# Kernel optimization log

Hardware: AMD Instinct MI355X
Metric: run time of the kernel (lower is better)

The kernel has to match this reference:

```python
import jax, jax.numpy as jnp
import numpy as np

COMMITMENT_COST = 0.25
K = 512  # code_book_dim
D = 64   # embedding_dim
N = 262144


def setup_inputs() -> dict:
    key = jax.random.key(0)
    k1, k2 = jax.random.split(key)
    inputs = jax.random.normal(k1, (N, D), dtype=jnp.float32)
    # torch init: uniform_(-1/K, 1/K)
    codebook = jax.random.uniform(k2, (K, D), dtype=jnp.float32, minval=-1.0 / K, maxval=1.0 / K)
    return {"inputs": inputs, "codebook": codebook}


def reference(inputs, codebook):
    flat = inputs  # [N, D]
    x_sq = jnp.sum(flat * flat, axis=1, keepdims=True)          # [N, 1]
    e_sq = jnp.sum(codebook * codebook, axis=1)[None, :]        # [1, K]
    distances = x_sq + e_sq - 2.0 * flat @ codebook.T           # [N, K]
    encoding_indices = jnp.argmin(distances, axis=1)            # [N]
    quantized = codebook[encoding_indices]                      # [N, D]

    e_latent_loss = jnp.mean((jax.lax.stop_gradient(quantized) - flat) ** 2)
    q_latent_loss = jnp.mean((quantized - jax.lax.stop_gradient(flat)) ** 2)
    loss = q_latent_loss + COMMITMENT_COST * e_latent_loss

    # training-mode straight-through estimator
    quantized_st = flat + jax.lax.stop_gradient(quantized - flat)
    return loss, quantized_st, encoding_indices
```

## Files before the change

### kernel.cpp

```cpp
#include <hip/hip_runtime.h>
#include <hip/hip_bf16.h>

#define N_ROWS 262144
#define DIM 64
#define KC 512
#define BLK 512
#define RPT 2
#define LDS_FLOATS (KC * DIM + KC)


__device__ __forceinline__ float np_sumsq64(const float* a) {
#pragma clang fp contract(off)
    float r[8];
#pragma unroll
    for (int j = 0; j < 8; ++j) r[j] = a[j] * a[j];
#pragma unroll
    for (int i = 8; i < 64; i += 8)
#pragma unroll
        for (int j = 0; j < 8; ++j) r[j] = r[j] + a[i + j] * a[i + j];
    return ((r[0] + r[1]) + (r[2] + r[3])) + ((r[4] + r[5]) + (r[6] + r[7]));
}

__global__ void esq_kernel(const float* __restrict__ cb, float* __restrict__ esq) {
    int k = blockIdx.x * blockDim.x + threadIdx.x;
    if (k < KC) esq[k] = np_sumsq64(cb + k * DIM);
}

__global__ __launch_bounds__(BLK)
__attribute__((amdgpu_waves_per_eu(2, 2)))
void vq_kernel(
    const float* __restrict__ x, const float* __restrict__ cb,
    const float* __restrict__ esq_g, float* __restrict__ out,
    float* __restrict__ loss_acc)
{
    extern __shared__ float smem[];
    float* cbs  = smem;
    float* esql = smem + KC * DIM;

    const int tid  = threadIdx.x;
    const int lane = tid & 63;
    const int row0 = blockIdx.x * (BLK * RPT) + tid;
    const int row1 = row0 + BLK;

    {
        const float4* g4 = reinterpret_cast<const float4*>(cb);
        float4*       s4 = reinterpret_cast<float4*>(cbs);
#pragma unroll
        for (int i = 0; i < (KC * DIM / 4) / BLK; ++i)
            s4[tid + i * BLK] = g4[tid + i * BLK];
        if (tid < KC) esql[tid] = esq_g[tid];
    }

    float xr0[DIM], xr1[DIM];
    {
        const float4* xv0 = reinterpret_cast<const float4*>(x + (size_t)row0 * DIM);
        const float4* xv1 = reinterpret_cast<const float4*>(x + (size_t)row1 * DIM);
#pragma unroll
        for (int j = 0; j < DIM / 4; ++j) {
            float4 v0 = xv0[j], v1 = xv1[j];
            xr0[4 * j + 0] = v0.x; xr0[4 * j + 1] = v0.y;
            xr0[4 * j + 2] = v0.z; xr0[4 * j + 3] = v0.w;
            xr1[4 * j + 0] = v1.x; xr1[4 * j + 1] = v1.y;
            xr1[4 * j + 2] = v1.z; xr1[4 * j + 3] = v1.w;
        }
    }

    const float xsq0 = np_sumsq64(xr0);
    const float xsq1 = np_sumsq64(xr1);

    __syncthreads();

    float best0 = 3.4e38f, best1 = 3.4e38f;
    int bidx0 = 0, bidx1 = 0;
#pragma unroll 1
    for (int k = 0; k < KC; k += 2) {
        const float4* ea = reinterpret_cast<const float4*>(cbs + k * DIM);
        const float4* eb = ea + DIM / 4;
        float dot00 = 0.f, dot01 = 0.f, dot10 = 0.f, dot11 = 0.f;
#pragma unroll
        for (int c = 0; c < DIM / 4; ++c) {
            const float4 a = ea[c];
            const float4 b = eb[c];
            dot00 = fmaf(xr0[4 * c + 0], a.x, dot00);
            dot01 = fmaf(xr0[4 * c + 0], b.x, dot01);
            dot10 = fmaf(xr1[4 * c + 0], a.x, dot10);
            dot11 = fmaf(xr1[4 * c + 0], b.x, dot11);
            dot00 = fmaf(xr0[4 * c + 1], a.y, dot00);
            dot01 = fmaf(xr0[4 * c + 1], b.y, dot01);
            dot10 = fmaf(xr1[4 * c + 1], a.y, dot10);
            dot11 = fmaf(xr1[4 * c + 1], b.y, dot11);
            dot00 = fmaf(xr0[4 * c + 2], a.z, dot00);
            dot01 = fmaf(xr0[4 * c + 2], b.z, dot01);
            dot10 = fmaf(xr1[4 * c + 2], a.z, dot10);
            dot11 = fmaf(xr1[4 * c + 2], b.z, dot11);
            dot00 = fmaf(xr0[4 * c + 3], a.w, dot00);
            dot01 = fmaf(xr0[4 * c + 3], b.w, dot01);
            dot10 = fmaf(xr1[4 * c + 3], a.w, dot10);
            dot11 = fmaf(xr1[4 * c + 3], b.w, dot11);
        }
        float d00, d01, d10, d11;
        {
#pragma clang fp contract(off)
            const float e0 = esql[k + 0], e1 = esql[k + 1];
            d00 = (xsq0 + e0) - 2.0f * dot00;
            d01 = (xsq0 + e1) - 2.0f * dot01;
            d10 = (xsq1 + e0) - 2.0f * dot10;
            d11 = (xsq1 + e1) - 2.0f * dot11;
        }
        if (d00 < best0) { best0 = d00; bidx0 = k + 0; }
        if (d01 < best0) { best0 = d01; bidx0 = k + 1; }
        if (d10 < best1) { best1 = d10; bidx1 = k + 0; }
        if (d11 < best1) { best1 = d11; bidx1 = k + 1; }
    }

    const size_t wave_row0 = (size_t)row0 - lane;
#pragma unroll 4
    for (int l = 0; l < 64; ++l) {
        const int idx = __shfl(bidx0, l, 64);
        out[1 + (wave_row0 + l) * DIM + lane] = cbs[idx * DIM + lane];
    }
    const size_t wave_row1 = (size_t)row1 - lane;
#pragma unroll 4
    for (int l = 0; l < 64; ++l) {
        const int idx = __shfl(bidx1, l, 64);
        out[1 + (wave_row1 + l) * DIM + lane] = cbs[idx * DIM + lane];
    }

    out[1 + (size_t)N_ROWS * DIM + row0] = (float)bidx0;
    out[1 + (size_t)N_ROWS * DIM + row1] = (float)bidx1;

    float lrow = best0 + best1;
#pragma unroll
    for (int off = 32; off > 0; off >>= 1) lrow += __shfl_down(lrow, off, 64);
    if (lane == 0) atomicAdd(loss_acc, lrow);
}

__global__ void fin_kernel(const float* __restrict__ loss_acc,
                           float* __restrict__ out) {
    if (threadIdx.x == 0) {
        float mean_sq = (*loss_acc) / (float)((size_t)N_ROWS * DIM);
        out[0] = 1.25f * mean_sq;
    }
}

extern "C" void kernel_launch(void* const* d_in, const int* in_sizes, int n_in,
                              void* d_out, int out_size, void* d_ws, size_t ws_size,
                              hipStream_t stream) {
    const float* x  = (const float*)d_in[0];
    const float* cb = (const float*)d_in[1];
    float* out = (float*)d_out;

    float* loss_acc = (float*)d_ws;
    float* esq      = (float*)((char*)d_ws + 256);

    hipMemsetAsync(d_ws, 0, 4, stream);
    esq_kernel<<<2, 256, 0, stream>>>(cb, esq);
    vq_kernel<<<N_ROWS / (BLK * RPT), BLK, LDS_FLOATS * sizeof(float), stream>>>(
        x, cb, esq, out, loss_acc);
    fin_kernel<<<1, 64, 0, stream>>>(loss_acc, out);
}
```

Measured before the change: 341.9 us.

## Split codebook search across two blocks per row chunk and combine results

Splits the 512-entry codebook into two halves, each handled by a separate block, so every block needs half the LDS. This doubles the grid and allows more resident waves per EU, raising occupancy. A new combine kernel picks the better partial result per row, gathers the codebook row from global memory, writes the outputs and accumulates the loss. In exchange, x is read twice and partial results take an extra workspace round trip, plus one more kernel launch.

```diff
diff --git a/kernel.cpp b/kernel.cpp
--- a/kernel.cpp
+++ b/kernel.cpp
@@ -4,9 +4,10 @@
 #define N_ROWS 262144
 #define DIM 64
 #define KC 512
+#define KHALF 256
 #define BLK 512
 #define RPT 2
-#define LDS_FLOATS (KC * DIM + KC)
+#define LDS_FLOATS (KHALF * DIM + KHALF)
 
 
 __device__ __forceinline__ float np_sumsq64(const float* a) {
@@ -27,28 +28,32 @@
 }
 
 __global__ __launch_bounds__(BLK)
-__attribute__((amdgpu_waves_per_eu(2, 2)))
-void vq_kernel(
+__attribute__((amdgpu_waves_per_eu(4, 4)))
+void vq_partial(
     const float* __restrict__ x, const float* __restrict__ cb,
-    const float* __restrict__ esq_g, float* __restrict__ out,
-    float* __restrict__ loss_acc)
+    const float* __restrict__ esq_g,
+    float* __restrict__ pbest, float* __restrict__ pidx)
 {
     extern __shared__ float smem[];
     float* cbs  = smem;
-    float* esql = smem + KC * DIM;
+    float* esql = smem + KHALF * DIM;
 
-    const int tid  = threadIdx.x;
-    const int lane = tid & 63;
-    const int row0 = blockIdx.x * (BLK * RPT) + tid;
-    const int row1 = row0 + BLK;
+    const int bid   = blockIdx.x;
+    const int half  = bid & 1;
+    const int chunk = bid >> 1;
+    const int tid   = threadIdx.x;
+    const int lane  = tid & 63;
+    const int row0  = chunk * (BLK * RPT) + tid;
+    const int row1  = row0 + BLK;
+    const int kbase = half * KHALF;
 
     {
-        const float4* g4 = reinterpret_cast<const float4*>(cb);
+        const float4* g4 = reinterpret_cast<const float4*>(cb + (size_t)kbase * DIM);
         float4*       s4 = reinterpret_cast<float4*>(cbs);
 #pragma unroll
-        for (int i = 0; i < (KC * DIM / 4) / BLK; ++i)
+        for (int i = 0; i < (KHALF * DIM / 4) / BLK; ++i)
             s4[tid + i * BLK] = g4[tid + i * BLK];
-        if (tid < KC) esql[tid] = esq_g[tid];
+        if (tid < KHALF) esql[tid] = esq_g[kbase + tid];
     }
 
     float xr0[DIM], xr1[DIM];
@@ -73,7 +78,7 @@
     float best0 = 3.4e38f, best1 = 3.4e38f;
     int bidx0 = 0, bidx1 = 0;
 #pragma unroll 1
-    for (int k = 0; k < KC; k += 2) {
+    for (int k = 0; k < KHALF; k += 2) {
         const float4* ea = reinterpret_cast<const float4*>(cbs + k * DIM);
         const float4* eb = ea + DIM / 4;
         float dot00 = 0.f, dot01 = 0.f, dot10 = 0.f, dot11 = 0.f;
@@ -113,23 +118,36 @@
         if (d11 < best1) { best1 = d11; bidx1 = k + 1; }
     }
 
-    const size_t wave_row0 = (size_t)row0 - lane;
+    const size_t po = (size_t)half * N_ROWS;
+    pbest[po + row0] = best0;
+    pbest[po + row1] = best1;
+    pidx [po + row0] = (float)(kbase + bidx0);
+    pidx [po + row1] = (float)(kbase + bidx1);
+}
+
+__global__ __launch_bounds__(256) void combine_kernel(
+    const float* __restrict__ cb,
+    const float* __restrict__ pbest, const float* __restrict__ pidx,
+    float* __restrict__ out, float* __restrict__ loss_acc)
+{
+    const int r    = blockIdx.x * 256 + threadIdx.x;
+    const int lane = threadIdx.x & 63;
+
+    const float bA = pbest[r], bB = pbest[N_ROWS + r];
+    float best = bA;
+    int   bidx = (int)pidx[r];
+    if (bB < bA) { best = bB; bidx = (int)pidx[N_ROWS + r]; }
+
+    const size_t wave_r0 = (size_t)r - lane;
 #pragma unroll 4
     for (int l = 0; l < 64; ++l) {
-        const int idx = __shfl(bidx0, l, 64);
-        out[1 + (wave_row0 + l) * DIM + lane] = cbs[idx * DIM + lane];
-    }
-    const size_t wave_row1 = (size_t)row1 - lane;
-#pragma unroll 4
-    for (int l = 0; l < 64; ++l) {
-        const int idx = __shfl(bidx1, l, 64);
-        out[1 + (wave_row1 + l) * DIM + lane] = cbs[idx * DIM + lane];
+        const int idx = __shfl(bidx, l, 64);
+        out[1 + (wave_r0 + l) * DIM + lane] = cb[(size_t)idx * DIM + lane];
     }
 
-    out[1 + (size_t)N_ROWS * DIM + row0] = (float)bidx0;
-    out[1 + (size_t)N_ROWS * DIM + row1] = (float)bidx1;
+    out[1 + (size_t)N_ROWS * DIM + r] = (float)bidx;
 
-    float lrow = best0 + best1;
+    float lrow = best;
 #pragma unroll
     for (int off = 32; off > 0; off >>= 1) lrow += __shfl_down(lrow, off, 64);
     if (lane == 0) atomicAdd(loss_acc, lrow);
@@ -152,10 +170,13 @@
 
     float* loss_acc = (float*)d_ws;
     float* esq      = (float*)((char*)d_ws + 256);
+    float* pbest    = (float*)((char*)d_ws + 4096);
+    float* pidx     = pbest + 2 * (size_t)N_ROWS;
 
     hipMemsetAsync(d_ws, 0, 4, stream);
     esq_kernel<<<2, 256, 0, stream>>>(cb, esq);
-    vq_kernel<<<N_ROWS / (BLK * RPT), BLK, LDS_FLOATS * sizeof(float), stream>>>(
-        x, cb, esq, out, loss_acc);
+    vq_partial<<<2 * (N_ROWS / (BLK * RPT)), BLK, LDS_FLOATS * sizeof(float), stream>>>(
+        x, cb, esq, pbest, pidx);
+    combine_kernel<<<N_ROWS / 256, 256, 0, stream>>>(cb, pbest, pidx, out, loss_acc);
     fin_kernel<<<1, 64, 0, stream>>>(loss_acc, out);
 }
```

Result: slower. 708.8 us (+107.3%).
